# Performance work log

Hardware: AMD Instinct MI355X
Metric: run time of the kernel (lower is better)

## Reference

```python
import jax, jax.numpy as jnp
import numpy as np

EPS = 1e-5

def _ternary(w):
    # BitNet 1.58-bit: per-output-channel scale = median(|W|) (scale_op='median'),
    # quantize to {-1,0,1}*scale with straight-through estimator.
    s = jnp.maximum(jnp.median(jnp.abs(w), axis=(1, 2, 3), keepdims=True), EPS)
    q = jnp.clip(jnp.round(w / s), -1.0, 1.0) * s
    return w + jax.lax.stop_gradient(q - w)

def _conv3x3(x, w):
    # NCHW, OIHW, stride 1, pad 1 (spatial-preserving)
    return jax.lax.conv_general_dilated(
        x, _ternary(w), (1, 1), ((1, 1), (1, 1)),
        dimension_numbers=('NCHW', 'OIHW', 'NCHW'))

def _bn(y, g, b, m, v):
    # eval-mode BatchNorm2d folded to a single scale/shift
    inv = g / jnp.sqrt(v + EPS)
    return y * inv[None, :, None, None] + (b - m * inv)[None, :, None, None]

def _ssh(x, p):
    (w3, g3, b3, m3, v3,
     ws, gs, bs, ms, vs,
     w5, g5, b5, m5, v5,
     w7a, g7a, b7a, m7a, v7a,
     w7b, g7b, b7b, m7b, v7b) = p
    c3 = _bn(_conv3x3(x, w3), g3, b3, m3, v3)                      # [B, half, H, W]
    stem = jax.nn.silu(_bn(_conv3x3(x, ws), gs, bs, ms, vs))       # [B, quart, H, W]
    c5 = _bn(_conv3x3(stem, w5), g5, b5, m5, v5)                   # [B, quart, H, W]
    t = jax.nn.silu(_bn(_conv3x3(stem, w7a), g7a, b7a, m7a, v7a))
    c7 = _bn(_conv3x3(t, w7b), g7b, b7b, m7b, v7b)                 # [B, quart, H, W]
    return jax.nn.silu(jnp.concatenate((c3, c5, c7), axis=1))      # [B, out_ch, H, W]

def setup_inputs() -> dict:
    key = jax.random.key(0)
    B, CIN, H, W = 32, 256, 64, 64
    HALF, Q = 128, 64  # out_ch=256 -> half=128, quart=64
    d = {"x": jax.random.normal(jax.random.fold_in(key, 0), (B, CIN, H, W), jnp.float32)}

    def mk(i, o, c):
        k0, k1, k2, k3, k4 = jax.random.split(jax.random.fold_in(key, i), 5)
        return (jax.random.normal(k0, (o, c, 3, 3), jnp.float32) * 0.05,
                1.0 + 0.1 * jax.random.normal(k1, (o,), jnp.float32),   # gamma
                0.1 * jax.random.normal(k2, (o,), jnp.float32),          # beta
                0.1 * jax.random.normal(k3, (o,), jnp.float32),          # running mean
                0.5 + jax.random.uniform(k4, (o,), jnp.float32))         # running var > 0

    for name, (o, c), i in [("3", (HALF, CIN), 1), ("s", (Q, CIN), 2),
                            ("5", (Q, Q), 3), ("7a", (Q, Q), 4), ("7b", (Q, Q), 5)]:
        w, g, b, m, v = mk(i, o, c)
        d["w" + name] = w; d["g" + name] = g; d["b" + name] = b
        d["m" + name] = m; d["v" + name] = v
    return d

def reference(x,
              w3, g3, b3, m3, v3,
              ws, gs, bs, ms, vs,
              w5, g5, b5, m5, v5,
              w7a, g7a, b7a, m7a, v7a,
              w7b, g7b, b7b, m7b, v7b):
    return _ssh(x, (w3, g3, b3, m3, v3, ws, gs, bs, ms, vs,
                    w5, g5, b5, m5, v5, w7a, g7a, b7a, m7a, v7a,
                    w7b, g7b, b7b, m7b, v7b))
```

## Files before the change

kernel.cpp:

```cpp
#include <hip/hip_runtime.h>
#include <stdint.h>

#define EPSF 1e-5f

typedef __bf16 bf16;
typedef __attribute__((ext_vector_type(8))) __bf16 bf16x8;
typedef __attribute__((ext_vector_type(4))) float f32x4;

#define GL16(src, dst) __builtin_amdgcn_global_load_lds( \
    (const __attribute__((address_space(1))) void*)(src), \
    (__attribute__((address_space(3))) void*)(dst), 16, 0, 0)
#define MEMFENCE() asm volatile("" ::: "memory")

template<int N> __device__ __forceinline__ void vwait() {
  static_assert(N == 2 || N == 4 || N == 6, "unsupported vmcnt");
  if constexpr (N == 2) asm volatile("s_waitcnt vmcnt(2)" ::: "memory");
  else if constexpr (N == 4) asm volatile("s_waitcnt vmcnt(4)" ::: "memory");
  else asm volatile("s_waitcnt vmcnt(6)" ::: "memory");
}

struct QArgs {
  const float* w[5];
  const float* g[5];
  const float* bb[5];
  const float* m[5];
  const float* v[5];
  bf16* wpk[3];
  float* alpha[3];
  float* beta[3];
};

__global__ __launch_bounds__(256)
void quant_kernel(QArgs qa) {
  __shared__ int red[2][4];
  const int tid = threadIdx.x;
  const int blk = blockIdx.x;
  int layer, o;
  if (blk < 128)      { layer = 0; o = blk; }
  else if (blk < 192) { layer = 1; o = blk - 128; }
  else if (blk < 256) { layer = 2; o = blk - 192; }
  else if (blk < 320) { layer = 3; o = blk - 256; }
  else                { layer = 4; o = blk - 320; }
  const int I_[5]     = {256, 256, 64, 64, 64};
  const int gemm_[5]  = {0, 0, 1, 1, 2};
  const int obase_[5] = {0, 128, 0, 64, 0};
  const int gNMT[3]   = {12, 8, 4};
  const int I = I_[layer];
  const int n = I * 9;
  const float* w = qa.w[layer] + (size_t)o * n;

  unsigned key[9];
#pragma unroll
  for (int j = 0; j < 9; ++j) key[j] = 0xFFFFFFFFu;
  {
    int c2 = 0;
    for (int i = tid; i < n; i += 256) key[c2++] = __float_as_uint(fabsf(w[i]));
  }

  const int wv = tid >> 6;
  unsigned pfx[2] = {0u, 0u};
  const int rank0 = n / 2 - 1, rank1 = n / 2;
  int pp = 0;
  for (int bit = 31; bit >= 0; --bit) {
    const unsigned c0 = pfx[0] | (1u << bit);
    const unsigned c1 = pfx[1] | (1u << bit);
    int loc = 0;
#pragma unroll
    for (int j = 0; j < 9; ++j)
      loc += (key[j] < c0 ? 1 : 0) + (key[j] < c1 ? 0x10000 : 0);
    loc += __shfl_xor(loc, 32); loc += __shfl_xor(loc, 16);
    loc += __shfl_xor(loc, 8);  loc += __shfl_xor(loc, 4);
    loc += __shfl_xor(loc, 2);  loc += __shfl_xor(loc, 1);
    if ((tid & 63) == 0) red[pp][wv] = loc;
    __syncthreads();
    const int tot = red[pp][0] + red[pp][1] + red[pp][2] + red[pp][3];
    if ((tot & 0xFFFF) <= rank0) pfx[0] = c0;
    if ((tot >> 16)    <= rank1) pfx[1] = c1;
    pp ^= 1;
  }
  const float s =
      fmaxf(0.5f * (__uint_as_float(pfx[0]) + __uint_as_float(pfx[1])), EPSF);

  const int g  = gemm_[layer];
  const int ob = obase_[layer];
  const int NMT = gNMT[g];
  if (tid == 0) {
    float inv = qa.g[layer][o] / sqrtf(qa.v[layer][o] + EPSF);
    qa.alpha[g][ob + o] = s * inv;
    qa.beta[g][ob + o]  = qa.bb[layer][o] - qa.m[layer][o] * inv;
  }
  const int og  = ob + o;
  const int mt  = og >> 4;
  const int l16 = og & 15;
  bf16* wp = qa.wpk[g];
  for (int i = tid; i < n; i += 256) {
    float t = rintf(w[i] / s);
    t = fmaxf(-1.f, fminf(1.f, t));
    int c = i / 9, pos = i % 9;
    int k = pos * I + c;
    int ks = k >> 5, kq = (k >> 3) & 3, jj = k & 7;
    wp[((size_t)((ks * NMT + mt) * 64 + kq * 16 + l16)) * 8 + jj] = (bf16)t;
  }
}

__global__ __launch_bounds__(256)
void transpose_k(const float* __restrict__ x, bf16* __restrict__ xT,
                 float* __restrict__ zp) {
  if (blockIdx.x == 0 && threadIdx.x < 32) zp[threadIdx.x] = 0.0f;
  __shared__ float tile[64 * 66];
  const int tid = threadIdx.x;
  const int blk = blockIdx.x;
  const int cg = blk & 3;
  const int h  = (blk >> 2) & 63;
  const int b  = blk >> 8;
  const int w4 = (tid & 15) * 4;
  const int cb = tid >> 4;
#pragma unroll
  for (int p = 0; p < 4; ++p) {
    int c = cb + p * 16;
    const float4 v =
        *(const float4*)&x[(((size_t)(b * 256 + cg * 64 + c)) * 64 + h) * 64 + w4];
    tile[(w4 + 0) * 66 + c] = v.x;
    tile[(w4 + 1) * 66 + c] = v.y;
    tile[(w4 + 2) * 66 + c] = v.z;
    tile[(w4 + 3) * 66 + c] = v.w;
  }
  __syncthreads();
#pragma unroll
  for (int p = 0; p < 2; ++p) {
    int id = tid + p * 256;
    int c8 = id & 7, w2 = id >> 3;
    const float* src = &tile[w2 * 66 + c8 * 8];
    float2 f0 = *(const float2*)(src + 0);
    float2 f1 = *(const float2*)(src + 2);
    float2 f2 = *(const float2*)(src + 4);
    float2 f3 = *(const float2*)(src + 6);
    bf16x8 v;
    v[0] = (bf16)f0.x; v[1] = (bf16)f0.y; v[2] = (bf16)f1.x; v[3] = (bf16)f1.y;
    v[4] = (bf16)f2.x; v[5] = (bf16)f2.y; v[6] = (bf16)f3.x; v[7] = (bf16)f3.y;
    *(bf16x8*)&xT[(((size_t)(b * 64 + h)) * 64 + w2) * 256 + cg * 64 + c8 * 8] = v;
  }
}

template<int CIN, int NMT, int MM, int C1, bool HASPAD>
__global__ __launch_bounds__(1024, 4)
void conv_k(const bf16* __restrict__ xin,
            const bf16* __restrict__ wpk,
            const float* __restrict__ alpha,
            const float* __restrict__ beta,
            float* __restrict__ out, int chan_off,
            bf16* __restrict__ padout,
            const bf16* __restrict__ zpage) {
  constexpr int NC = CIN / 32;
  __shared__ __align__(16) union U {
    bf16 xs[2][12800];
    bf16 ep[256 * 72];
  } sm;

  const int tid  = threadIdx.x;
  const int wave = tid >> 6;
  const int lane = tid & 63;
  const int q    = lane >> 4;
  const int t16  = lane & 15;
  const int rw   = wave >> 2;
  const int mt0  = (wave & 3) * MM;
  const int wg   = (int)blockIdx.x;
  const int wgid = (wg & 7) * 64 + (wg >> 3);
  const int b    = wgid >> 4;
  const int h0   = (wgid & 15) << 2;

  const bf16* srcp[2];
  int step[2];
#pragma unroll
  for (int p = 0; p < 2; ++p) {
    const int id = tid + p * 1024;
    const int c8p = id & 3, rj = id >> 2;
    const int j = rj % 66, r = rj / 66;
    const int hh = h0 + r - 1, ww = j - 1;
    const bool v = (id < 1584) && ((unsigned)hh < 64u) && ((unsigned)ww < 64u);
    const int c8 = c8p ^ ((j >> 1) & 3);
    srcp[p] = v ? &xin[(((size_t)(b * 64 + hh)) * 64 + ww) * CIN + c8 * 8] : zpage;
    step[p] = v ? 32 : 0;
  }

  int Caddr[3];
#pragma unroll
  for (int kw = 0; kw < 3; ++kw) {
    const int col = t16 + kw;
    Caddr[kw] = rw * 4224 + col * 64 + ((q ^ ((col >> 1) & 3)) << 4);
  }

  char* const lds0 = (char*)&sm.xs[0][0];

  GL16(srcp[0], lds0 + wave * 1024);
  if (wave < 9) GL16(srcp[1], lds0 + 16384 + wave * 1024);
  if constexpr (NC == 2) {
    GL16(srcp[0] + step[0], lds0 + 25600 + wave * 1024);
    if (wave < 9) GL16(srcp[1] + step[1], lds0 + 25600 + 16384 + wave * 1024);
  } else {
#pragma unroll
    for (int p = 0; p < 2; ++p) srcp[p] += step[p];
  }
  MEMFENCE();

  bf16x8 fr[3][MM];
#pragma unroll
  for (int mm = 0; mm < MM; ++mm) {
    fr[0][mm] = *(const bf16x8*)&wpk[((size_t)(mt0 + mm) * 64 + lane) * 8];
    fr[1][mm] = *(const bf16x8*)&wpk[((size_t)(NC * NMT + mt0 + mm) * 64 + lane) * 8];
  }

  f32x4 acc[4][MM] = {};
  int tog = 25600;

  for (int ci = 0; ci < NC; ++ci) {
    if (NC > 2 || ci == 0) {
      vwait<2 * MM>();
      __builtin_amdgcn_s_barrier();
    }
    if constexpr (NC > 2) {
      if (ci + 1 < NC) {
        char* lb = lds0 + (((ci + 1) & 1) ? 25600 : 0);
        GL16(srcp[0], lb + wave * 1024);
        if (wave < 9) GL16(srcp[1], lb + 16384 + wave * 1024);
#pragma unroll
        for (int p = 0; p < 2; ++p) srcp[p] += step[p];
      }
    }
    MEMFENCE();
    __builtin_amdgcn_s_setprio(1);
#pragma unroll
    for (int pos = 0; pos < 9; ++pos) {
      const int t = pos + 2;
      if (t <= 8) {
        const int ksn = t * NC + ci;
#pragma unroll
        for (int mm = 0; mm < MM; ++mm)
          fr[t % 3][mm] = *(const bf16x8*)&wpk[((size_t)(ksn * NMT + mt0 + mm) * 64 + lane) * 8];
      } else if (ci + 1 < NC) {
        const int ksn = (t - 9) * NC + (ci + 1);
#pragma unroll
        for (int mm = 0; mm < MM; ++mm)
          fr[t % 3][mm] = *(const bf16x8*)&wpk[((size_t)(ksn * NMT + mt0 + mm) * 64 + lane) * 8];
      }
      const int kh = pos / 3, kw = pos % 3;
#pragma unroll
      for (int nt = 0; nt < 4; ++nt) {
        const bf16x8 bv =
            *(const bf16x8*)(lds0 + (Caddr[kw] + nt * 1024 + kh * 4224));
#pragma unroll
        for (int mm = 0; mm < MM; ++mm)
          acc[nt][mm] = __builtin_amdgcn_mfma_f32_16x16x32_bf16(fr[pos % 3][mm], bv, acc[nt][mm], 0, 0, 0);
      }
    }
    __builtin_amdgcn_s_setprio(0);
#pragma unroll
    for (int kw = 0; kw < 3; ++kw) Caddr[kw] += tog;
    tog = -tog;
  }

  const int h = h0 + rw;
#pragma unroll
  for (int mm = 0; mm < MM; ++mm) {
    const int o0 = (mt0 + mm) * 16 + 4 * q;
    float av[4], bv2[4];
#pragma unroll
    for (int i = 0; i < 4; ++i) { av[i] = alpha[o0 + i]; bv2[i] = beta[o0 + i]; }
#pragma unroll
    for (int nt = 0; nt < 4; ++nt) {
      const int wv = nt * 16 + t16;
#pragma unroll
      for (int i = 0; i < 4; ++i) {
        float v = acc[nt][mm][i] * av[i] + bv2[i];
        float sg = v / (1.f + __expf(-v));
        acc[nt][mm][i] = sg;
        if (o0 < C1)
          out[(((size_t)(b * 256 + chan_off + o0 + i)) * 64 + h) * 64 + wv] = sg;
      }
    }
  }
  if (HASPAD) {
    __syncthreads();
#pragma unroll
    for (int mm = 0; mm < MM; ++mm) {
      const int o0 = (mt0 + mm) * 16 + 4 * q;
      if (o0 >= C1) {
#pragma unroll
        for (int nt = 0; nt < 4; ++nt) {
          const int px = rw * 64 + nt * 16 + t16;
          union { bf16 h4[4]; uint2 u; } pk;
#pragma unroll
          for (int i = 0; i < 4; ++i) pk.h4[i] = (bf16)acc[nt][mm][i];
          *(uint2*)&sm.ep[px * 72 + (o0 - C1)] = pk.u;
        }
      }
    }
    __syncthreads();
#pragma unroll
    for (int p = 0; p < 2; ++p) {
      int id = tid + p * 1024;
      int c8 = id & 7, px = id >> 3;
      bf16x8 v = *(const bf16x8*)&sm.ep[px * 72 + c8 * 8];
      const int r = px >> 6, wv2 = px & 63;
      *(bf16x8*)&padout[(((size_t)(b * 64 + h0 + r)) * 64 + wv2) * 64 + c8 * 8] = v;
    }
  }
}

extern "C" void kernel_launch(void* const* d_in, const int* in_sizes, int n_in,
                              void* d_out, int out_size, void* d_ws, size_t ws_size,
                              hipStream_t stream) {
  QArgs qa;
  const float* x = (const float*)d_in[0];
  for (int L = 0; L < 5; ++L) {
    qa.w[L]  = (const float*)d_in[1 + 5 * L];
    qa.g[L]  = (const float*)d_in[2 + 5 * L];
    qa.bb[L] = (const float*)d_in[3 + 5 * L];
    qa.m[L]  = (const float*)d_in[4 + 5 * L];
    qa.v[L]  = (const float*)d_in[5 + 5 * L];
  }
  char* p = (char*)d_ws;
  bf16* wpk1 = (bf16*)p; p += (size_t)192 * 2304 * 2;
  bf16* wpk2 = (bf16*)p; p += (size_t)128 * 576 * 2;
  bf16* wpk3 = (bf16*)p; p += (size_t)64 * 576 * 2;
  float* a1 = (float*)p; p += 1024;
  float* b1 = (float*)p; p += 1024;
  float* a2 = (float*)p; p += 1024;
  float* b2 = (float*)p; p += 1024;
  float* a3 = (float*)p; p += 1024;
  float* b3 = (float*)p; p += 1024;
  float* zp = (float*)p; p += 128;
  bf16* xT   = (bf16*)p; p += (size_t)32 * 64 * 64 * 256 * 2;
  bf16* stem = (bf16*)p; p += (size_t)32 * 64 * 64 * 64 * 2;
  bf16* tbuf = xT;
  qa.wpk[0] = wpk1; qa.wpk[1] = wpk2; qa.wpk[2] = wpk3;
  qa.alpha[0] = a1; qa.alpha[1] = a2; qa.alpha[2] = a3;
  qa.beta[0]  = b1; qa.beta[1]  = b2; qa.beta[2]  = b3;

  quant_kernel<<<384, 256, 0, stream>>>(qa);
  transpose_k<<<32 * 64 * 4, 256, 0, stream>>>(x, xT, zp);

  const bf16* zpb = (const bf16*)zp;
  conv_k<256, 12, 3, 128, true ><<<512, 1024, 0, stream>>>(xT,   wpk1, a1, b1, (float*)d_out, 0,   stem, zpb);
  conv_k< 64,  8, 2,  64, true ><<<512, 1024, 0, stream>>>(stem, wpk2, a2, b2, (float*)d_out, 128, tbuf, zpb);
  conv_k< 64,  4, 1,  64, false><<<512, 1024, 0, stream>>>(tbuf, wpk3, a3, b3, (float*)d_out, 192, nullptr, zpb);
}
```

Before: 440.2 us.

## Parametrize conv tile rows and block size; use smaller blocks for first and last convs

Generalizes the conv kernel over threads per block, rows per block, and an optional block-index swizzle. The first conv now uses 512-thread blocks covering 2 output rows (1024 blocks), and the last conv uses 512 threads with MM=2 over 4 rows. Staging loops and the epilogue are rewritten generically. The intent is better occupancy and load balance through smaller LDS footprints and more blocks, at the cost of more halo reloads per output row for the 2-row tiles.

```diff
diff --git a/kernel.cpp b/kernel.cpp
--- a/kernel.cpp
+++ b/kernel.cpp
@@ -142,8 +142,8 @@
   }
 }
 
-template<int CIN, int NMT, int MM, int C1, bool HASPAD>
-__global__ __launch_bounds__(1024, 4)
+template<int CIN, int NMT, int MM, int C1, bool HASPAD, int TPB, int RB, bool XSWZ>
+__global__ __launch_bounds__(TPB, 4)
 void conv_k(const bf16* __restrict__ xin,
             const bf16* __restrict__ wpk,
             const float* __restrict__ alpha,
@@ -151,10 +151,19 @@
             float* __restrict__ out, int chan_off,
             bf16* __restrict__ padout,
             const bf16* __restrict__ zpage) {
-  constexpr int NC = CIN / 32;
+  constexpr int NC    = CIN / 32;
+  constexpr int NG    = NMT / MM;
+  constexpr int RS    = RB + 2;
+  constexpr int NCHK  = RS * 66 * 4;
+  constexpr int SLOTS = (RB == 2) ? 1088 : 1600;
+  constexpr int BUFB  = SLOTS * 16;
+  constexpr int P     = (NCHK + TPB - 1) / TPB;
+  constexpr int HT    = 64 / RB;
+  constexpr int NBLK  = 32 * HT;
+
   __shared__ __align__(16) union U {
-    bf16 xs[2][12800];
-    bf16 ep[256 * 72];
+    bf16 xs[2][SLOTS * 8];
+    bf16 ep[RB * 64 * 72];
   } sm;
 
   const int tid  = threadIdx.x;
@@ -162,27 +171,35 @@
   const int lane = tid & 63;
   const int q    = lane >> 4;
   const int t16  = lane & 15;
-  const int rw   = wave >> 2;
-  const int mt0  = (wave & 3) * MM;
+  const int rw   = wave / NG;
+  const int mt0  = (wave % NG) * MM;
   const int wg   = (int)blockIdx.x;
-  const int wgid = (wg & 7) * 64 + (wg >> 3);
-  const int b    = wgid >> 4;
-  const int h0   = (wgid & 15) << 2;
-
-  const bf16* srcp[2];
-  int step[2];
-#pragma unroll
-  for (int p = 0; p < 2; ++p) {
-    const int id = tid + p * 1024;
+  const int wgid = XSWZ ? (wg & 7) * (NBLK / 8) + (wg >> 3) : wg;
+  const int b    = wgid / HT;
+  const int h0   = (wgid % HT) * RB;
+
+  const bf16* srcp[P];
+  int step[P];
+#pragma unroll
+  for (int p = 0; p < P; ++p) {
+    const int id = tid + p * TPB;
     const int c8p = id & 3, rj = id >> 2;
     const int j = rj % 66, r = rj / 66;
     const int hh = h0 + r - 1, ww = j - 1;
-    const bool v = (id < 1584) && ((unsigned)hh < 64u) && ((unsigned)ww < 64u);
+    const bool v = (id < NCHK) && ((unsigned)hh < 64u) && ((unsigned)ww < 64u);
     const int c8 = c8p ^ ((j >> 1) & 3);
     srcp[p] = v ? &xin[(((size_t)(b * 64 + hh)) * 64 + ww) * CIN + c8 * 8] : zpage;
     step[p] = v ? 32 : 0;
   }
 
+  auto stage = [&](char* base, bool second) {
+#pragma unroll
+    for (int p = 0; p < P; ++p) {
+      if ((p + 1) * TPB <= NCHK || p * TPB + wave * 64 < NCHK)
+        GL16(srcp[p] + (second ? step[p] : 0), base + (p * TPB + wave * 64) * 16);
+    }
+  };
+
   int Caddr[3];
 #pragma unroll
   for (int kw = 0; kw < 3; ++kw) {
@@ -192,14 +209,12 @@
 
   char* const lds0 = (char*)&sm.xs[0][0];
 
-  GL16(srcp[0], lds0 + wave * 1024);
-  if (wave < 9) GL16(srcp[1], lds0 + 16384 + wave * 1024);
+  stage(lds0, false);
   if constexpr (NC == 2) {
-    GL16(srcp[0] + step[0], lds0 + 25600 + wave * 1024);
-    if (wave < 9) GL16(srcp[1] + step[1], lds0 + 25600 + 16384 + wave * 1024);
+    stage(lds0 + BUFB, true);
   } else {
 #pragma unroll
-    for (int p = 0; p < 2; ++p) srcp[p] += step[p];
+    for (int p = 0; p < P; ++p) srcp[p] += step[p];
   }
   MEMFENCE();
 
@@ -211,7 +226,7 @@
   }
 
   f32x4 acc[4][MM] = {};
-  int tog = 25600;
+  int tog = BUFB;
 
   for (int ci = 0; ci < NC; ++ci) {
     if (NC > 2 || ci == 0) {
@@ -220,11 +235,9 @@
     }
     if constexpr (NC > 2) {
       if (ci + 1 < NC) {
-        char* lb = lds0 + (((ci + 1) & 1) ? 25600 : 0);
-        GL16(srcp[0], lb + wave * 1024);
-        if (wave < 9) GL16(srcp[1], lb + 16384 + wave * 1024);
-#pragma unroll
-        for (int p = 0; p < 2; ++p) srcp[p] += step[p];
+        stage(lds0 + (((ci + 1) & 1) ? BUFB : 0), false);
+#pragma unroll
+        for (int p = 0; p < P; ++p) srcp[p] += step[p];
       }
     }
     MEMFENCE();
@@ -296,9 +309,10 @@
       }
     }
     __syncthreads();
-#pragma unroll
-    for (int p = 0; p < 2; ++p) {
-      int id = tid + p * 1024;
+    constexpr int EPP = (RB * 64 * 8) / TPB;
+#pragma unroll
+    for (int p = 0; p < EPP; ++p) {
+      int id = tid + p * TPB;
       int c8 = id & 7, px = id >> 3;
       bf16x8 v = *(const bf16x8*)&sm.ep[px * 72 + c8 * 8];
       const int r = px >> 6, wv2 = px & 63;
@@ -341,7 +355,7 @@
   transpose_k<<<32 * 64 * 4, 256, 0, stream>>>(x, xT, zp);
 
   const bf16* zpb = (const bf16*)zp;
-  conv_k<256, 12, 3, 128, true ><<<512, 1024, 0, stream>>>(xT,   wpk1, a1, b1, (float*)d_out, 0,   stem, zpb);
-  conv_k< 64,  8, 2,  64, true ><<<512, 1024, 0, stream>>>(stem, wpk2, a2, b2, (float*)d_out, 128, tbuf, zpb);
-  conv_k< 64,  4, 1,  64, false><<<512, 1024, 0, stream>>>(tbuf, wpk3, a3, b3, (float*)d_out, 192, nullptr, zpb);
-}
+  conv_k<256, 12, 3, 128, true,  512, 2, false><<<1024,  512, 0, stream>>>(xT,   wpk1, a1, b1, (float*)d_out, 0,   stem, zpb);
+  conv_k< 64,  8, 2,  64, true, 1024, 4, true ><<< 512, 1024, 0, stream>>>(stem, wpk2, a2, b2, (float*)d_out, 128, tbuf, zpb);
+  conv_k< 64,  4, 2,  64, false, 512, 4, true ><<< 512,  512, 0, stream>>>(tbuf, wpk3, a3, b3, (float*)d_out, 192, nullptr, zpb);
+}
```

Result: no change. 435.2 us (-1.1%).
